# Kernel optimization log

Measured on AMD Instinct MI355X. Metric: run time of the kernel, lower is better.

## Reference

```python
import jax, jax.numpy as jnp
import numpy as np

N_NODES = 50000
N_EDGES = 800000
DIM = 128
NEG_SLOPE = 0.01  # nn.LeakyReLU default


def setup_inputs() -> dict:
    key = jax.random.key(0)
    ks = jax.random.split(key, 9)
    src = jax.random.randint(ks[0], (N_EDGES,), 0, N_NODES, dtype=jnp.int32)
    dst = jax.random.randint(ks[1], (N_EDGES,), 0, N_NODES, dtype=jnp.int32)
    weight = jax.random.normal(ks[2], (N_NODES,), dtype=jnp.float32)
    significance = jax.random.randint(ks[3], (N_NODES,), 0, 2, dtype=jnp.int32)
    emb = jax.random.normal(ks[4], (2, 2), dtype=jnp.float32) * 0.1
    W0 = jax.random.normal(ks[5], (3, DIM), dtype=jnp.float32) * (1.0 / np.sqrt(3))
    b0 = jnp.zeros((DIM,), dtype=jnp.float32)
    W1 = jax.random.normal(ks[6], (DIM, DIM), dtype=jnp.float32) * (1.0 / np.sqrt(DIM))
    b1 = jnp.zeros((DIM,), dtype=jnp.float32)
    return {"src": src, "dst": dst, "weight": weight, "significance": significance,
            "emb": emb, "W0": W0, "b0": b0, "W1": W1, "b1": b1}


def _graph_conv(src, dst, x, W, b, n_nodes):
    # DGL GraphConv, norm='both', allow_zero_in_degree=True:
    # h = D_in^{-1/2} A D_out^{-1/2} x W + b, degrees clamped to >= 1.
    ones = jnp.ones(src.shape[0], dtype=x.dtype)
    out_deg = jnp.clip(jax.ops.segment_sum(ones, src, num_segments=n_nodes), 1.0)
    in_deg = jnp.clip(jax.ops.segment_sum(ones, dst, num_segments=n_nodes), 1.0)
    h = x * (out_deg ** -0.5)[:, None]            # [N, d] scale src side
    agg = jax.ops.segment_sum(h[src], dst, num_segments=n_nodes)  # gather+scatter over edges
    agg = agg * (in_deg ** -0.5)[:, None]
    return agg @ W + b


def reference(src, dst, weight, significance, emb, W0, b0, W1, b1):
    n_nodes = weight.shape[0]
    sig = emb[significance]                        # [N, 2] embedding lookup
    feats = jnp.concatenate([weight[:, None], sig], axis=1)  # [N, 3]
    h = _graph_conv(src, dst, feats, W0, b0, n_nodes)        # conv_0
    h = jax.nn.leaky_relu(h, negative_slope=NEG_SLOPE)
    h = _graph_conv(src, dst, h, W1, b1, n_nodes)            # layers[0]
    return h
```

## Files before the change

### kernel.cpp

```cpp
#include <hip/hip_runtime.h>

#define N_NODES 50000
#define N_EDGES 800000
#define DIM 128
#define NEG_SLOPE 0.01f
#define CAP 32
#define OVF_MAX 4096

#define NR 4
#define RNODES 12512
#define SLICES 64
#define ESLICE (N_EDGES / SLICES)

__device__ inline unsigned f2b_rne2(float a, float b) {
    unsigned ua = __float_as_uint(a), ub = __float_as_uint(b);
    ua = (ua + 0x7fffu + ((ua >> 16) & 1u)) >> 16;
    ub = (ub + 0x7fffu + ((ub >> 16) & 1u)) >> 16;
    return ua | (ub << 16);
}
__device__ inline float b2f_lo(unsigned u) { return __uint_as_float(u << 16); }
__device__ inline float b2f_hi(unsigned u) { return __uint_as_float(u & 0xffff0000u); }

__global__ void k_fillbucket(const int* __restrict__ src, const int* __restrict__ dst,
                             int* __restrict__ icnt,
                             unsigned short* __restrict__ eidx,
                             int* __restrict__ ovf_cnt, int2* __restrict__ ovf, int ne2) {
    int t = blockIdx.x * blockDim.x + threadIdx.x;
    if (t >= ne2) return;
    int2 s = ((const int2*)src)[t];
    int2 d = ((const int2*)dst)[t];
    int p0 = atomicAdd(&icnt[d.x], 1);
    if (p0 < CAP) eidx[d.x * CAP + p0] = (unsigned short)s.x;
    else { int o = atomicAdd(ovf_cnt, 1); if (o < OVF_MAX) ovf[o] = make_int2(d.x, s.x); }
    int p1 = atomicAdd(&icnt[d.y], 1);
    if (p1 < CAP) eidx[d.y * CAP + p1] = (unsigned short)s.y;
    else { int o = atomicAdd(ovf_cnt, 1); if (o < OVF_MAX) ovf[o] = make_int2(d.y, s.y); }
}

__global__ __launch_bounds__(256) void k_hist(const int* __restrict__ src,
                                              int* __restrict__ partial) {
    __shared__ int bins[RNODES];
    int range = blockIdx.x / SLICES;
    int slice = blockIdx.x % SLICES;
    int tid = threadIdx.x;
    for (int j = tid; j < RNODES; j += 256) bins[j] = 0;
    __syncthreads();
    int base_node = range * RNODES;
    const int4* src4 = (const int4*)(src + slice * ESLICE);
    for (int t = tid; t < ESLICE / 4; t += 256) {
        int4 v = src4[t];
        unsigned u0 = (unsigned)(v.x - base_node);
        unsigned u1 = (unsigned)(v.y - base_node);
        unsigned u2 = (unsigned)(v.z - base_node);
        unsigned u3 = (unsigned)(v.w - base_node);
        if (u0 < RNODES) atomicAdd(&bins[u0], 1);
        if (u1 < RNODES) atomicAdd(&bins[u1], 1);
        if (u2 < RNODES) atomicAdd(&bins[u2], 1);
        if (u3 < RNODES) atomicAdd(&bins[u3], 1);
    }
    __syncthreads();
    int* outp = partial + (size_t)blockIdx.x * RNODES;
    for (int j = tid; j < RNODES; j += 256) outp[j] = bins[j];
}

__global__ void k_prep(const float* __restrict__ weight, const int* __restrict__ sig,
                       const float* __restrict__ emb,
                       const int* __restrict__ partial, const int* __restrict__ icnt,
                       float* __restrict__ oinv, float* __restrict__ iinv,
                       float* __restrict__ feats3, int n) {
    int i = blockIdx.x * blockDim.x + threadIdx.x;
    if (i >= n) return;
    int range = i / RNODES, off = i % RNODES;
    const int* p = partial + ((size_t)range * SLICES) * RNODES + off;
    int od = 0;
    #pragma unroll 8
    for (int s = 0; s < SLICES; ++s) od += p[(size_t)s * RNODES];
    float odf = (float)max(od, 1);
    float idf = (float)max(icnt[i], 1);
    float oi = 1.0f / sqrtf(odf);
    oinv[i] = oi;
    iinv[i] = 1.0f / sqrtf(idf);
    int sg = sig[i];
    feats3[i * 3 + 0] = weight[i] * oi;
    feats3[i * 3 + 1] = emb[sg * 2 + 0] * oi;
    feats3[i * 3 + 2] = emb[sg * 2 + 1] * oi;
}

__global__ void k_ovf3(const int* __restrict__ ovf_cnt, const int2* __restrict__ ovf,
                       const float* __restrict__ feats3, float* __restrict__ agg3ovf) {
    int t = blockIdx.x * blockDim.x + threadIdx.x;
    int cnt = min(*ovf_cnt, OVF_MAX);
    if (t >= cnt) return;
    int2 e = ovf[t];
    atomicAdd(&agg3ovf[e.x * 3 + 0], feats3[e.y * 3 + 0]);
    atomicAdd(&agg3ovf[e.x * 3 + 1], feats3[e.y * 3 + 1]);
    atomicAdd(&agg3ovf[e.x * 3 + 2], feats3[e.y * 3 + 2]);
}

__global__ void k_aggl1(const int* __restrict__ icnt, const unsigned short* __restrict__ eidx,
                        const float* __restrict__ feats3, const float* __restrict__ agg3ovf,
                        const float* __restrict__ iinv, const float* __restrict__ oinv,
                        const float* __restrict__ W0, const float* __restrict__ b0,
                        unsigned* __restrict__ hs, int n) {
    int t = blockIdx.x * blockDim.x + threadIdx.x;
    int i = t >> 5;
    if (i >= n) return;
    int q = t & 31;
    int deg = min(icnt[i], CAP);
    const unsigned short* row = eidx + i * CAP;
    float a0 = 0.f, a1 = 0.f, a2 = 0.f;
    for (int k = q; k < deg; k += 32) {
        int s = row[k];
        a0 += feats3[s * 3 + 0];
        a1 += feats3[s * 3 + 1];
        a2 += feats3[s * 3 + 2];
    }
    #pragma unroll
    for (int m = 1; m <= 16; m <<= 1) {
        a0 += __shfl_xor(a0, m);
        a1 += __shfl_xor(a1, m);
        a2 += __shfl_xor(a2, m);
    }
    a0 += agg3ovf[i * 3 + 0];
    a1 += agg3ovf[i * 3 + 1];
    a2 += agg3ovf[i * 3 + 2];
    float ii = iinv[i], oi = oinv[i];
    a0 *= ii; a1 *= ii; a2 *= ii;
    int j0 = q * 4;
    float4 w0r = *(const float4*)&W0[0 * DIM + j0];
    float4 w1r = *(const float4*)&W0[1 * DIM + j0];
    float4 w2r = *(const float4*)&W0[2 * DIM + j0];
    float4 bb  = *(const float4*)&b0[j0];
    float v0 = a0 * w0r.x + a1 * w1r.x + a2 * w2r.x + bb.x;
    float v1 = a0 * w0r.y + a1 * w1r.y + a2 * w2r.y + bb.y;
    float v2 = a0 * w0r.z + a1 * w1r.z + a2 * w2r.z + bb.z;
    float v3 = a0 * w0r.w + a1 * w1r.w + a2 * w2r.w + bb.w;
    v0 = v0 > 0.f ? v0 : NEG_SLOPE * v0;
    v1 = v1 > 0.f ? v1 : NEG_SLOPE * v1;
    v2 = v2 > 0.f ? v2 : NEG_SLOPE * v2;
    v3 = v3 > 0.f ? v3 : NEG_SLOPE * v3;
    ((uint2*)hs)[i * 32 + q] = make_uint2(f2b_rne2(v0 * oi, v1 * oi),
                                          f2b_rne2(v2 * oi, v3 * oi));
}

__global__ void k_gather128(const int* __restrict__ icnt, const unsigned short* __restrict__ eidx,
                            const unsigned* __restrict__ hs, float* __restrict__ agg, int n) {
    int t = blockIdx.x * blockDim.x + threadIdx.x;
    int i = t >> 5;
    if (i >= n) return;
    int q = t & 31;
    int deg = min(icnt[i], CAP);
    const unsigned short* row = eidx + i * CAP;
    const uint2* hs2 = (const uint2*)hs;
    float a0 = 0.f, a1 = 0.f, a2 = 0.f, a3 = 0.f;
    int k = 0;
    for (; k + 2 <= deg; k += 2) {
        int s0 = row[k], s1 = row[k + 1];
        uint2 u0 = hs2[s0 * 32 + q];
        uint2 u1 = hs2[s1 * 32 + q];
        a0 += b2f_lo(u0.x) + b2f_lo(u1.x);
        a1 += b2f_hi(u0.x) + b2f_hi(u1.x);
        a2 += b2f_lo(u0.y) + b2f_lo(u1.y);
        a3 += b2f_hi(u0.y) + b2f_hi(u1.y);
    }
    if (k < deg) {
        int s = row[k];
        uint2 u = hs2[s * 32 + q];
        a0 += b2f_lo(u.x); a1 += b2f_hi(u.x);
        a2 += b2f_lo(u.y); a3 += b2f_hi(u.y);
    }
    ((float4*)agg)[i * 32 + q] = make_float4(a0, a1, a2, a3);
}

__global__ void k_overflow(const int* __restrict__ ovf_cnt, const int2* __restrict__ ovf,
                           const unsigned* __restrict__ hs, float* __restrict__ agg) {
    int g = blockIdx.x * blockDim.x + threadIdx.x;
    int entry = g >> 5, q = g & 31;
    int cnt = min(*ovf_cnt, OVF_MAX);
    if (entry >= cnt) return;
    int2 e = ovf[entry];
    uint2 u = ((const uint2*)hs)[e.y * 32 + q];
    float* o = agg + (size_t)e.x * DIM + q * 4;
    atomicAdd(o + 0, b2f_lo(u.x));
    atomicAdd(o + 1, b2f_hi(u.x));
    atomicAdd(o + 2, b2f_lo(u.y));
    atomicAdd(o + 3, b2f_hi(u.y));
}

#define FB_NODES 256
__global__ __launch_bounds__(256) void k_final(const float* __restrict__ iinv,
                                               const float* __restrict__ W1,
                                               const float* __restrict__ b1,
                                               const float* __restrict__ agg,
                                               float* __restrict__ out, int n) {
    __shared__ float sW[DIM * 64];
    int tid = threadIdx.x;
    int half = blockIdx.x & 1;
    int tile = blockIdx.x >> 1;
    for (int idx = tid; idx < DIM * 64 / 4; idx += 256) {
        int r = idx >> 4, c4 = idx & 15;
        *(float4*)&sW[r * 64 + c4 * 4] = *(const float4*)&W1[r * DIM + half * 64 + c4 * 4];
    }
    int cg = tid & 7;
    int ng = tid >> 3;
    int col0 = cg * 8;
    int row0 = tile * FB_NODES + ng * 8;

    float acc[8][8];
    #pragma unroll
    for (int i = 0; i < 8; ++i)
        #pragma unroll
        for (int j = 0; j < 8; ++j) acc[i][j] = 0.f;

    __syncthreads();

    const float4* agg4 = (const float4*)agg;
    for (int k4 = 0; k4 < 32; ++k4) {
        float4 a[8];
        #pragma unroll
        for (int i = 0; i < 8; ++i) {
            int r = min(row0 + i, n - 1);
            a[i] = agg4[(size_t)r * 32 + k4];
        }
        #pragma unroll
        for (int kk = 0; kk < 4; ++kk) {
            float4 w0 = *(const float4*)&sW[(k4 * 4 + kk) * 64 + col0];
            float4 w1v = *(const float4*)&sW[(k4 * 4 + kk) * 64 + col0 + 4];
            #pragma unroll
            for (int i = 0; i < 8; ++i) {
                float av = (kk == 0) ? a[i].x : (kk == 1) ? a[i].y : (kk == 2) ? a[i].z : a[i].w;
                acc[i][0] += av * w0.x;  acc[i][1] += av * w0.y;
                acc[i][2] += av * w0.z;  acc[i][3] += av * w0.w;
                acc[i][4] += av * w1v.x; acc[i][5] += av * w1v.y;
                acc[i][6] += av * w1v.z; acc[i][7] += av * w1v.w;
            }
        }
    }

    int gcol = half * 64 + col0;
    float4 bb0 = *(const float4*)&b1[gcol];
    float4 bb1 = *(const float4*)&b1[gcol + 4];
    #pragma unroll
    for (int i = 0; i < 8; ++i) {
        int r = row0 + i;
        if (r < n) {
            float ii = iinv[r];
            float4 o0, o1;
            o0.x = acc[i][0] * ii + bb0.x; o0.y = acc[i][1] * ii + bb0.y;
            o0.z = acc[i][2] * ii + bb0.z; o0.w = acc[i][3] * ii + bb0.w;
            o1.x = acc[i][4] * ii + bb1.x; o1.y = acc[i][5] * ii + bb1.y;
            o1.z = acc[i][6] * ii + bb1.z; o1.w = acc[i][7] * ii + bb1.w;
            ((float4*)out)[(size_t)r * 32 + (gcol >> 2)] = o0;
            ((float4*)out)[(size_t)r * 32 + (gcol >> 2) + 1] = o1;
        }
    }
}

extern "C" void kernel_launch(void* const* d_in, const int* in_sizes, int n_in,
                              void* d_out, int out_size, void* d_ws, size_t ws_size,
                              hipStream_t stream) {
    const int*   src  = (const int*)d_in[0];
    const int*   dst  = (const int*)d_in[1];
    const float* weight = (const float*)d_in[2];
    const int*   sig  = (const int*)d_in[3];
    const float* emb  = (const float*)d_in[4];
    const float* W0   = (const float*)d_in[5];
    const float* b0   = (const float*)d_in[6];
    const float* W1   = (const float*)d_in[7];
    const float* b1   = (const float*)d_in[8];
    float* out = (float*)d_out;

    int*   icnt    = (int*)d_ws;
    int*   ovf_cnt = icnt + N_NODES;
    float* agg3ovf = (float*)(ovf_cnt + 8);
    int2*  ovf     = (int2*)(agg3ovf + 3 * N_NODES);
    float* oinv    = (float*)(ovf + OVF_MAX);
    float* iinv    = oinv + N_NODES;
    float* feats3  = iinv + N_NODES;
    int*   partial = (int*)(feats3 + 3 * N_NODES);
    unsigned short* eidx = (unsigned short*)(partial + (size_t)NR * SLICES * RNODES);
    unsigned* hs   = (unsigned*)(eidx + (size_t)N_NODES * CAP);
    float* aggbuf  = (float*)(hs + (size_t)N_NODES * 64);

    hipMemsetAsync(d_ws, 0, (size_t)(N_NODES + 8 + 3 * N_NODES) * 4, stream);

    k_fillbucket<<<(N_EDGES / 2 + 255) / 256, 256, 0, stream>>>(src, dst, icnt, eidx,
                                                                ovf_cnt, ovf, N_EDGES / 2);
    k_hist<<<NR * SLICES, 256, 0, stream>>>(src, partial);
    k_prep<<<(N_NODES + 255) / 256, 256, 0, stream>>>(weight, sig, emb, partial, icnt,
                                                      oinv, iinv, feats3, N_NODES);
    k_ovf3<<<(OVF_MAX + 255) / 256, 256, 0, stream>>>(ovf_cnt, ovf, feats3, agg3ovf);
    k_aggl1<<<(N_NODES * 32 + 255) / 256, 256, 0, stream>>>(icnt, eidx, feats3, agg3ovf,
                                                            iinv, oinv, W0, b0, hs, N_NODES);
    k_gather128<<<((N_NODES * 32) + 255) / 256, 256, 0, stream>>>(icnt, eidx, hs, aggbuf,
                                                                  N_NODES);
    k_overflow<<<(OVF_MAX * 32) / 256, 256, 0, stream>>>(ovf_cnt, ovf, hs, aggbuf);
    k_final<<<((N_NODES + FB_NODES - 1) / FB_NODES) * 2, 256, 0, stream>>>(
        iinv, W1, b1, aggbuf, out, N_NODES);
}
```

Measured before the change: 156.7 us.

## Replace global-atomic bucket fill with shared-memory histogram, scan, and slice fill

Edge bucketing no longer uses global atomics on a per-node counter. Source and destination degrees are now histogrammed together in LDS per (range, slice) block. A per-node scan over slices turns the destination counts into starting offsets, and a third kernel places each edge's source into eidx using LDS atomics seeded from those offsets. This removes contended global atomics and gives a deterministic slot order, at the cost of extra passes that re-read src/dst and write and read a second partial-count array.

```diff
diff --git a/kernel.cpp b/kernel.cpp
--- a/kernel.cpp
+++ b/kernel.cpp
@@ -21,69 +21,98 @@
 __device__ inline float b2f_lo(unsigned u) { return __uint_as_float(u << 16); }
 __device__ inline float b2f_hi(unsigned u) { return __uint_as_float(u & 0xffff0000u); }
 
-__global__ void k_fillbucket(const int* __restrict__ src, const int* __restrict__ dst,
-                             int* __restrict__ icnt,
-                             unsigned short* __restrict__ eidx,
-                             int* __restrict__ ovf_cnt, int2* __restrict__ ovf, int ne2) {
-    int t = blockIdx.x * blockDim.x + threadIdx.x;
-    if (t >= ne2) return;
-    int2 s = ((const int2*)src)[t];
-    int2 d = ((const int2*)dst)[t];
-    int p0 = atomicAdd(&icnt[d.x], 1);
-    if (p0 < CAP) eidx[d.x * CAP + p0] = (unsigned short)s.x;
-    else { int o = atomicAdd(ovf_cnt, 1); if (o < OVF_MAX) ovf[o] = make_int2(d.x, s.x); }
-    int p1 = atomicAdd(&icnt[d.y], 1);
-    if (p1 < CAP) eidx[d.y * CAP + p1] = (unsigned short)s.y;
-    else { int o = atomicAdd(ovf_cnt, 1); if (o < OVF_MAX) ovf[o] = make_int2(d.y, s.y); }
-}
-
-__global__ __launch_bounds__(256) void k_hist(const int* __restrict__ src,
-                                              int* __restrict__ partial) {
-    __shared__ int bins[RNODES];
+__global__ __launch_bounds__(512) void k_hist2(const int* __restrict__ src,
+                                               const int* __restrict__ dst,
+                                               int* __restrict__ pSrc, int* __restrict__ pDst) {
+    __shared__ int bs[RNODES];
+    __shared__ int bd[RNODES];
     int range = blockIdx.x / SLICES;
     int slice = blockIdx.x % SLICES;
     int tid = threadIdx.x;
-    for (int j = tid; j < RNODES; j += 256) bins[j] = 0;
+    for (int j = tid; j < RNODES; j += 512) { bs[j] = 0; bd[j] = 0; }
     __syncthreads();
-    int base_node = range * RNODES;
-    const int4* src4 = (const int4*)(src + slice * ESLICE);
-    for (int t = tid; t < ESLICE / 4; t += 256) {
-        int4 v = src4[t];
-        unsigned u0 = (unsigned)(v.x - base_node);
-        unsigned u1 = (unsigned)(v.y - base_node);
-        unsigned u2 = (unsigned)(v.z - base_node);
-        unsigned u3 = (unsigned)(v.w - base_node);
-        if (u0 < RNODES) atomicAdd(&bins[u0], 1);
-        if (u1 < RNODES) atomicAdd(&bins[u1], 1);
-        if (u2 < RNODES) atomicAdd(&bins[u2], 1);
-        if (u3 < RNODES) atomicAdd(&bins[u3], 1);
+    int base = range * RNODES;
+    const int4* s4 = (const int4*)(src + slice * ESLICE);
+    const int4* d4 = (const int4*)(dst + slice * ESLICE);
+    for (int t = tid; t < ESLICE / 4; t += 512) {
+        int4 v = s4[t];
+        unsigned u0 = (unsigned)(v.x - base), u1 = (unsigned)(v.y - base);
+        unsigned u2 = (unsigned)(v.z - base), u3 = (unsigned)(v.w - base);
+        if (u0 < RNODES) atomicAdd(&bs[u0], 1);
+        if (u1 < RNODES) atomicAdd(&bs[u1], 1);
+        if (u2 < RNODES) atomicAdd(&bs[u2], 1);
+        if (u3 < RNODES) atomicAdd(&bs[u3], 1);
+        int4 w = d4[t];
+        unsigned w0 = (unsigned)(w.x - base), w1 = (unsigned)(w.y - base);
+        unsigned w2 = (unsigned)(w.z - base), w3 = (unsigned)(w.w - base);
+        if (w0 < RNODES) atomicAdd(&bd[w0], 1);
+        if (w1 < RNODES) atomicAdd(&bd[w1], 1);
+        if (w2 < RNODES) atomicAdd(&bd[w2], 1);
+        if (w3 < RNODES) atomicAdd(&bd[w3], 1);
     }
     __syncthreads();
-    int* outp = partial + (size_t)blockIdx.x * RNODES;
-    for (int j = tid; j < RNODES; j += 256) outp[j] = bins[j];
-}
-
-__global__ void k_prep(const float* __restrict__ weight, const int* __restrict__ sig,
-                       const float* __restrict__ emb,
-                       const int* __restrict__ partial, const int* __restrict__ icnt,
-                       float* __restrict__ oinv, float* __restrict__ iinv,
-                       float* __restrict__ feats3, int n) {
-    int i = blockIdx.x * blockDim.x + threadIdx.x;
-    if (i >= n) return;
-    int range = i / RNODES, off = i % RNODES;
-    const int* p = partial + ((size_t)range * SLICES) * RNODES + off;
+    int* os = pSrc + (size_t)blockIdx.x * RNODES;
+    int* od = pDst + (size_t)blockIdx.x * RNODES;
+    for (int j = tid; j < RNODES; j += 512) { os[j] = bs[j]; od[j] = bd[j]; }
+}
+
+__global__ void k_scanprep(const float* __restrict__ weight, const int* __restrict__ sig,
+                           const float* __restrict__ emb,
+                           const int* __restrict__ pSrc, int* __restrict__ pDst,
+                           int* __restrict__ icnt, float* __restrict__ oinv,
+                           float* __restrict__ iinv, float* __restrict__ feats3, int n) {
+    int g = blockIdx.x * blockDim.x + threadIdx.x;
+    if (g >= NR * RNODES) return;
+    int range = g / RNODES, off = g % RNODES;
+    size_t basei = (size_t)(range * SLICES) * RNODES + off;
+    int run = 0;
+    #pragma unroll 8
+    for (int s = 0; s < SLICES; ++s) {
+        size_t idx = basei + (size_t)s * RNODES;
+        int c = pDst[idx];
+        pDst[idx] = run;
+        run += c;
+    }
     int od = 0;
     #pragma unroll 8
-    for (int s = 0; s < SLICES; ++s) od += p[(size_t)s * RNODES];
-    float odf = (float)max(od, 1);
-    float idf = (float)max(icnt[i], 1);
-    float oi = 1.0f / sqrtf(odf);
-    oinv[i] = oi;
-    iinv[i] = 1.0f / sqrtf(idf);
-    int sg = sig[i];
-    feats3[i * 3 + 0] = weight[i] * oi;
-    feats3[i * 3 + 1] = emb[sg * 2 + 0] * oi;
-    feats3[i * 3 + 2] = emb[sg * 2 + 1] * oi;
+    for (int s = 0; s < SLICES; ++s) od += pSrc[basei + (size_t)s * RNODES];
+    if (g < n) {
+        icnt[g] = run;
+        float oi = 1.0f / sqrtf((float)max(od, 1));
+        oinv[g] = oi;
+        iinv[g] = 1.0f / sqrtf((float)max(run, 1));
+        int sg = sig[g];
+        feats3[g * 3 + 0] = weight[g] * oi;
+        feats3[g * 3 + 1] = emb[sg * 2 + 0] * oi;
+        feats3[g * 3 + 2] = emb[sg * 2 + 1] * oi;
+    }
+}
+
+__global__ __launch_bounds__(512) void k_fill3(const int* __restrict__ src,
+                                               const int* __restrict__ dst,
+                                               const int* __restrict__ pDst,
+                                               unsigned short* __restrict__ eidx,
+                                               int* __restrict__ ovf_cnt, int2* __restrict__ ovf) {
+    __shared__ int cur[RNODES];
+    int range = blockIdx.x / SLICES;
+    int slice = blockIdx.x % SLICES;
+    int tid = threadIdx.x;
+    const int* pr = pDst + (size_t)blockIdx.x * RNODES;
+    for (int j = tid; j < RNODES; j += 512) cur[j] = pr[j];
+    __syncthreads();
+    int base = range * RNODES;
+    const int* ss = src + slice * ESLICE;
+    const int* dd = dst + slice * ESLICE;
+    for (int t = tid; t < ESLICE; t += 512) {
+        int d = dd[t];
+        unsigned u = (unsigned)(d - base);
+        if (u < RNODES) {
+            int s = ss[t];
+            int p = atomicAdd(&cur[u], 1);
+            if (p < CAP) eidx[(size_t)d * CAP + p] = (unsigned short)s;
+            else { int o = atomicAdd(ovf_cnt, 1); if (o < OVF_MAX) ovf[o] = make_int2(d, s); }
+        }
+    }
 }
 
 __global__ void k_ovf3(const int* __restrict__ ovf_cnt, const int2* __restrict__ ovf,
@@ -270,25 +299,26 @@
     const float* b1   = (const float*)d_in[8];
     float* out = (float*)d_out;
 
-    int*   icnt    = (int*)d_ws;
-    int*   ovf_cnt = icnt + N_NODES;
+    int*   ovf_cnt = (int*)d_ws;
     float* agg3ovf = (float*)(ovf_cnt + 8);
     int2*  ovf     = (int2*)(agg3ovf + 3 * N_NODES);
-    float* oinv    = (float*)(ovf + OVF_MAX);
+    int*   icnt    = (int*)(ovf + OVF_MAX);
+    float* oinv    = (float*)(icnt + N_NODES);
     float* iinv    = oinv + N_NODES;
     float* feats3  = iinv + N_NODES;
-    int*   partial = (int*)(feats3 + 3 * N_NODES);
-    unsigned short* eidx = (unsigned short*)(partial + (size_t)NR * SLICES * RNODES);
+    int*   pSrc    = (int*)(feats3 + 3 * N_NODES);
+    int*   pDst    = pSrc + (size_t)NR * SLICES * RNODES;
+    unsigned short* eidx = (unsigned short*)(pDst + (size_t)NR * SLICES * RNODES);
     unsigned* hs   = (unsigned*)(eidx + (size_t)N_NODES * CAP);
     float* aggbuf  = (float*)(hs + (size_t)N_NODES * 64);
 
-    hipMemsetAsync(d_ws, 0, (size_t)(N_NODES + 8 + 3 * N_NODES) * 4, stream);
-
-    k_fillbucket<<<(N_EDGES / 2 + 255) / 256, 256, 0, stream>>>(src, dst, icnt, eidx,
-                                                                ovf_cnt, ovf, N_EDGES / 2);
-    k_hist<<<NR * SLICES, 256, 0, stream>>>(src, partial);
-    k_prep<<<(N_NODES + 255) / 256, 256, 0, stream>>>(weight, sig, emb, partial, icnt,
-                                                      oinv, iinv, feats3, N_NODES);
+    hipMemsetAsync(d_ws, 0, (size_t)(8 + 3 * N_NODES) * 4, stream);
+
+    k_hist2<<<NR * SLICES, 512, 0, stream>>>(src, dst, pSrc, pDst);
+    k_scanprep<<<(NR * RNODES + 255) / 256, 256, 0, stream>>>(weight, sig, emb, pSrc, pDst,
+                                                              icnt, oinv, iinv, feats3,
+                                                              N_NODES);
+    k_fill3<<<NR * SLICES, 512, 0, stream>>>(src, dst, pDst, eidx, ovf_cnt, ovf);
     k_ovf3<<<(OVF_MAX + 255) / 256, 256, 0, stream>>>(ovf_cnt, ovf, feats3, agg3ovf);
     k_aggl1<<<(N_NODES * 32 + 255) / 256, 256, 0, stream>>>(icnt, eidx, feats3, agg3ovf,
                                                             iinv, oinv, W0, b0, hs, N_NODES);
```

Result: faster. 142.4 us (-9.1%).
